# Performance work log

Hardware: AMD Instinct MI355X
Metric: run time of the kernel (lower is better)

The kernel has to match this reference:

```python
import jax, jax.numpy as jnp
import numpy as np

EMB_DIM = 1024
HID_DIM = 4096
NUM_EXPERTS = 8
TOPK = 2


def setup_inputs() -> dict:
    key = jax.random.key(0)
    ks = jax.random.split(key, 8)
    B, S, D, H, E = 4, 2048, EMB_DIM, HID_DIM, NUM_EXPERTS
    s_in = 1.0 / np.sqrt(D)
    s_hid = 1.0 / np.sqrt(H)
    x = jax.random.normal(ks[0], (B, S, D), dtype=jnp.float32)
    wr = jax.random.normal(ks[1], (D, E), dtype=jnp.float32) * s_in
    br = jnp.zeros((E,), dtype=jnp.float32)
    w1 = jax.random.normal(ks[2], (E, D, H), dtype=jnp.float32) * s_in
    b1 = jnp.zeros((E, H), dtype=jnp.float32)
    w2 = jax.random.normal(ks[3], (E, H, D), dtype=jnp.float32) * s_hid
    b2 = jnp.zeros((E, D), dtype=jnp.float32)
    return {"x": x, "wr": wr, "br": br, "w1": w1, "b1": b1, "w2": w2, "b2": b2}


def reference(x, wr, br, w1, b1, w2, b2):
    B, S, D = x.shape
    xf = x.reshape(-1, D)                                   # [T, D]
    logits = xf @ wr + br                                   # [T, E]
    probs = jax.nn.softmax(logits, axis=-1)                 # [T, E]
    _, topk_idx = jax.lax.top_k(probs, TOPK)                # [T, K]
    routed = jax.nn.one_hot(topk_idx, NUM_EXPERTS, dtype=probs.dtype).sum(axis=1)  # [T, E]
    gates = probs * routed                                  # zero for non-topk experts
    out = jnp.zeros_like(xf)
    for e in range(NUM_EXPERTS):                            # fixed small loop over experts
        h = jax.nn.relu(xf @ w1[e] + b1[e])                 # [T, H]
        y = h @ w2[e] + b2[e]                               # [T, D]
        out = out + gates[:, e:e + 1] * y
    return out.reshape(B, S, D)
```

## Files before the change

kernel.cpp:

```cpp
#include <hip/hip_runtime.h>
#include <hip/hip_bf16.h>
#include <stdint.h>


#define T_TOK 8192
#define D_DIM 1024
#define H_DIM 4096
#define NEXP  8
#define ROWCAP (T_TOK*2 + NEXP*128)

typedef short s16x8 __attribute__((ext_vector_type(8)));
typedef float f32x4 __attribute__((ext_vector_type(4)));

__device__ __forceinline__ unsigned short f2bf(float v) {
    __hip_bfloat16 b = __float2bfloat16(v);
    return __builtin_bit_cast(unsigned short, b);
}

__device__ __forceinline__ void gl_lds16(const unsigned short* g, unsigned short* l) {
    __builtin_amdgcn_global_load_lds((const __attribute__((address_space(1))) void*)g,
                                     (__attribute__((address_space(3))) void*)l, 16, 0, 0);
}


__global__ __launch_bounds__(256) void convx_kernel(const float* __restrict__ x,
                                                    unsigned short* __restrict__ xbf) {
    int i = blockIdx.x * 256 + threadIdx.x;
    float4 v = ((const float4*)x)[i];
    ushort4 o;
    o.x = f2bf(v.x); o.y = f2bf(v.y); o.z = f2bf(v.z); o.w = f2bf(v.w);
    ((ushort4*)xbf)[i] = o;
}

__global__ __launch_bounds__(256) void convt_kernel(const float* __restrict__ src,
                                                    unsigned short* __restrict__ dst,
                                                    int R, int C) {
    __shared__ float tile[32][33];
    size_t mat = (size_t)R * C;
    const float* s = src + (size_t)blockIdx.z * mat;
    unsigned short* d = dst + (size_t)blockIdx.z * mat;
    int c0 = blockIdx.x << 5, r0 = blockIdx.y << 5;
    int tx = threadIdx.x, ty = threadIdx.y;
#pragma unroll
    for (int i = 0; i < 4; i++)
        tile[ty + 8*i][tx] = s[(size_t)(r0 + ty + 8*i) * C + c0 + tx];
    __syncthreads();
#pragma unroll
    for (int i = 0; i < 4; i++)
        d[(size_t)(c0 + ty + 8*i) * R + r0 + tx] = f2bf(tile[tx][ty + 8*i]);
}


__global__ __launch_bounds__(256) void router_kernel(const float* __restrict__ x,
                                                     const float* __restrict__ wr,
                                                     const float* __restrict__ br,
                                                     int* __restrict__ counts,
                                                     int* __restrict__ te,
                                                     float* __restrict__ tg) {
    int wid = threadIdx.x >> 6, lane = threadIdx.x & 63;
    int t = blockIdx.x * 4 + wid;
    int g = lane >> 3;
    const float* xr = x + (size_t)t * D_DIM;
    float acc = 0.f;
#pragma unroll 8
    for (int j = 0; j < 128; j++)
        acc += xr[g + 8*j] * wr[lane + 64*j];
    acc += __shfl_xor(acc, 8);
    acc += __shfl_xor(acc, 16);
    acc += __shfl_xor(acc, 32);
    float lg[8];
#pragma unroll
    for (int q = 0; q < 8; q++) lg[q] = __shfl(acc, q) + br[q];
    if (lane == 0) {
        float mx = lg[0];
#pragma unroll
        for (int q = 1; q < 8; q++) mx = fmaxf(mx, lg[q]);
        float p[8], s = 0.f;
#pragma unroll
        for (int q = 0; q < 8; q++) { p[q] = __expf(lg[q] - mx); s += p[q]; }
        int i1 = 0;
#pragma unroll
        for (int q = 1; q < 8; q++) if (p[q] > p[i1]) i1 = q;
        int i2 = (i1 == 0) ? 1 : 0;
#pragma unroll
        for (int q = 0; q < 8; q++) if (q != i1 && p[q] > p[i2]) i2 = q;
        float inv = 1.f / s;
        atomicAdd(&counts[i1], 1);
        atomicAdd(&counts[i2], 1);
        te[t] = i1;          tg[t] = p[i1] * inv;
        te[T_TOK + t] = i2;  tg[T_TOK + t] = p[i2] * inv;
    }
}

__global__ void offsets_kernel(const int* __restrict__ counts, int* __restrict__ poff) {
    if (threadIdx.x == 0 && blockIdx.x == 0) {
        int acc = 0; poff[0] = 0;
#pragma unroll
        for (int e = 0; e < 8; e++) { acc += (counts[e] + 127) & ~127; poff[e + 1] = acc; }
    }
}

__global__ __launch_bounds__(256) void scatter_kernel(const int* __restrict__ te,
                                                      const float* __restrict__ tg,
                                                      int* __restrict__ counts2,
                                                      const int* __restrict__ poff,
                                                      int* __restrict__ list,
                                                      float* __restrict__ gate) {
    int i = blockIdx.x * 256 + threadIdx.x;
    if (i >= 2 * T_TOK) return;
    int e = te[i];
    int slot = atomicAdd(&counts2[e], 1);
    int gidx = poff[e] + slot;
    list[gidx] = i & (T_TOK - 1);
    gate[gidx] = tg[i];
}


__global__ __launch_bounds__(256) void ffn1_kernel(const unsigned short* __restrict__ xbf,
                                                   const unsigned short* __restrict__ w1t,
                                                   const float* __restrict__ b1,
                                                   unsigned short* __restrict__ hbuf,
                                                   const int* __restrict__ list,
                                                   const int* __restrict__ poff) {
    __shared__ unsigned short As[128 * 64];
    __shared__ unsigned short Bs[128 * 64];
    int row0 = blockIdx.x << 7;
    if (row0 >= poff[8]) return;
    int e = 0;
#pragma unroll
    for (int i = 1; i < 8; i++) e += (row0 >= poff[i]);
    const unsigned short* Bp = w1t + (size_t)e * D_DIM * H_DIM;
    int n0 = blockIdx.y << 7;
    int tid = threadIdx.x, lane = tid & 63, wid = tid >> 6;
    int wm = wid >> 1, wn = wid & 1;

    const unsigned short* asrc[4];
    const unsigned short* bsrc[4];
#pragma unroll
    for (int i = 0; i < 4; i++) {
        int lin = tid + (i << 8);
        int r = lin >> 3, kc = lin & 7;
        int tok = list[row0 + r];
        asrc[i] = xbf + (size_t)tok * D_DIM + kc * 8;
        bsrc[i] = Bp + (size_t)(n0 + r) * D_DIM + kc * 8;
    }
    f32x4 acc[4][4] = {};
    for (int k0 = 0; k0 < D_DIM; k0 += 64) {
        __syncthreads();
#pragma unroll
        for (int i = 0; i < 4; i++) {
            int lin = tid + (i << 8);
            gl_lds16(asrc[i] + k0, As + lin * 8);
            gl_lds16(bsrc[i] + k0, Bs + lin * 8);
        }
        __syncthreads();
#pragma unroll
        for (int kk = 0; kk < 64; kk += 32) {
            s16x8 af[4], bf_[4];
#pragma unroll
            for (int m = 0; m < 4; m++)
                af[m] = *(const s16x8*)(As + ((wm*64 + m*16 + (lane & 15)) * 64 + kk + (lane >> 4) * 8));
#pragma unroll
            for (int n = 0; n < 4; n++)
                bf_[n] = *(const s16x8*)(Bs + ((wn*64 + n*16 + (lane & 15)) * 64 + kk + (lane >> 4) * 8));
#pragma unroll
            for (int m = 0; m < 4; m++)
#pragma unroll
                for (int n = 0; n < 4; n++)
                    acc[m][n] = __builtin_amdgcn_mfma_f32_16x16x32_bf16(af[m], bf_[n], acc[m][n], 0, 0, 0);
        }
    }
#pragma unroll
    for (int m = 0; m < 4; m++) {
        int rbase = row0 + wm*64 + m*16 + ((lane >> 4) << 2);
#pragma unroll
        for (int n = 0; n < 4; n++) {
            int c = n0 + wn*64 + n*16 + (lane & 15);
            float bias = b1[e * H_DIM + c];
#pragma unroll
            for (int j = 0; j < 4; j++) {
                float v = fmaxf(acc[m][n][j] + bias, 0.0f);
                hbuf[(size_t)(rbase + j) * H_DIM + c] = f2bf(v);
            }
        }
    }
}

__global__ __launch_bounds__(256) void ffn2_kernel(const unsigned short* __restrict__ hbuf,
                                                   const unsigned short* __restrict__ w2t,
                                                   const float* __restrict__ b2,
                                                   float* __restrict__ out,
                                                   const int* __restrict__ list,
                                                   const float* __restrict__ gate,
                                                   const int* __restrict__ poff) {
    __shared__ unsigned short As[128 * 64];
    __shared__ unsigned short Bs[128 * 64];
    int row0 = blockIdx.x << 7;
    if (row0 >= poff[8]) return;
    int e = 0;
#pragma unroll
    for (int i = 1; i < 8; i++) e += (row0 >= poff[i]);
    const unsigned short* Bp = w2t + (size_t)e * D_DIM * H_DIM;
    int n0 = blockIdx.y << 7;
    int tid = threadIdx.x, lane = tid & 63, wid = tid >> 6;
    int wm = wid >> 1, wn = wid & 1;

    const unsigned short* asrc[4];
    const unsigned short* bsrc[4];
#pragma unroll
    for (int i = 0; i < 4; i++) {
        int lin = tid + (i << 8);
        int r = lin >> 3, kc = lin & 7;
        asrc[i] = hbuf + (size_t)(row0 + r) * H_DIM + kc * 8;
        bsrc[i] = Bp + (size_t)(n0 + r) * H_DIM + kc * 8;
    }
    f32x4 acc[4][4] = {};
    for (int k0 = 0; k0 < H_DIM; k0 += 64) {
        __syncthreads();
#pragma unroll
        for (int i = 0; i < 4; i++) {
            int lin = tid + (i << 8);
            gl_lds16(asrc[i] + k0, As + lin * 8);
            gl_lds16(bsrc[i] + k0, Bs + lin * 8);
        }
        __syncthreads();
#pragma unroll
        for (int kk = 0; kk < 64; kk += 32) {
            s16x8 af[4], bf_[4];
#pragma unroll
            for (int m = 0; m < 4; m++)
                af[m] = *(const s16x8*)(As + ((wm*64 + m*16 + (lane & 15)) * 64 + kk + (lane >> 4) * 8));
#pragma unroll
            for (int n = 0; n < 4; n++)
                bf_[n] = *(const s16x8*)(Bs + ((wn*64 + n*16 + (lane & 15)) * 64 + kk + (lane >> 4) * 8));
#pragma unroll
            for (int m = 0; m < 4; m++)
#pragma unroll
                for (int n = 0; n < 4; n++)
                    acc[m][n] = __builtin_amdgcn_mfma_f32_16x16x32_bf16(af[m], bf_[n], acc[m][n], 0, 0, 0);
        }
    }
#pragma unroll
    for (int m = 0; m < 4; m++) {
#pragma unroll
        for (int j = 0; j < 4; j++) {
            int srow = row0 + wm*64 + m*16 + ((lane >> 4) << 2) + j;
            float g = gate[srow];
            if (g != 0.0f) {
                int tok = list[srow];
#pragma unroll
                for (int n = 0; n < 4; n++) {
                    int c = n0 + wn*64 + n*16 + (lane & 15);
                    float v = g * (acc[m][n][j] + b2[e * D_DIM + c]);
                    atomicAdd(&out[(size_t)tok * D_DIM + c], v);
                }
            }
        }
    }
}


extern "C" void kernel_launch(void* const* d_in, const int* in_sizes, int n_in,
                              void* d_out, int out_size, void* d_ws, size_t ws_size,
                              hipStream_t stream) {
    const float* x  = (const float*)d_in[0];
    const float* wr = (const float*)d_in[1];
    const float* br = (const float*)d_in[2];
    const float* w1 = (const float*)d_in[3];
    const float* b1 = (const float*)d_in[4];
    const float* w2 = (const float*)d_in[5];
    const float* b2 = (const float*)d_in[6];
    float* out = (float*)d_out;
    (void)in_sizes; (void)n_in; (void)ws_size;

    char* ws = (char*)d_ws;
    size_t off = 0;
    auto alloc = [&](size_t bytes) { size_t o = off; off = (off + bytes + 1023) & ~(size_t)1023; return o; };
    size_t o_meta = alloc(256);
    size_t o_list = alloc((size_t)ROWCAP * 4);
    size_t o_gate = alloc((size_t)ROWCAP * 4);
    size_t o_te   = alloc((size_t)2 * T_TOK * 4);
    size_t o_tg   = alloc((size_t)2 * T_TOK * 4);
    size_t o_xbf  = alloc((size_t)T_TOK * D_DIM * 2);
    size_t o_w1t  = alloc((size_t)NEXP * D_DIM * H_DIM * 2);
    size_t o_w2t  = alloc((size_t)NEXP * D_DIM * H_DIM * 2);
    size_t o_h    = alloc((size_t)ROWCAP * H_DIM * 2);

    int* counts  = (int*)(ws + o_meta);
    int* counts2 = counts + 8;
    int* poff    = counts + 16;
    int* list    = (int*)(ws + o_list);
    float* gate  = (float*)(ws + o_gate);
    int* te      = (int*)(ws + o_te);
    float* tg    = (float*)(ws + o_tg);
    unsigned short* xbf = (unsigned short*)(ws + o_xbf);
    unsigned short* w1t = (unsigned short*)(ws + o_w1t);
    unsigned short* w2t = (unsigned short*)(ws + o_w2t);
    unsigned short* hbuf = (unsigned short*)(ws + o_h);

    hipMemsetAsync(ws + o_meta, 0, 256, stream);
    hipMemsetAsync(ws + o_list, 0, (size_t)ROWCAP * 4, stream);
    hipMemsetAsync(ws + o_gate, 0, (size_t)ROWCAP * 4, stream);
    hipMemsetAsync(d_out, 0, (size_t)out_size * 4, stream);

    convx_kernel<<<T_TOK * D_DIM / 4 / 256, 256, 0, stream>>>(x, xbf);
    convt_kernel<<<dim3(H_DIM / 32, D_DIM / 32, NEXP), dim3(32, 8), 0, stream>>>(w1, w1t, D_DIM, H_DIM);
    convt_kernel<<<dim3(D_DIM / 32, H_DIM / 32, NEXP), dim3(32, 8), 0, stream>>>(w2, w2t, H_DIM, D_DIM);

    router_kernel<<<T_TOK / 4, 256, 0, stream>>>(x, wr, br, counts, te, tg);
    offsets_kernel<<<1, 64, 0, stream>>>(counts, poff);
    scatter_kernel<<<(2 * T_TOK) / 256, 256, 0, stream>>>(te, tg, counts2, poff, list, gate);

    ffn1_kernel<<<dim3(ROWCAP / 128, H_DIM / 128), 256, 0, stream>>>(xbf, w1t, b1, hbuf, list, poff);
    ffn2_kernel<<<dim3(ROWCAP / 128, D_DIM / 128), 256, 0, stream>>>(hbuf, w2t, b2, out, list, gate, poff);
}
```

Measured before the change: 1.272 ms.

## Swizzle LDS tiles and replace atomic scatter with per-slot buffer plus combine

Applies an XOR swizzle to the LDS layout of the A and B tiles in both expert GEMMs, so the MFMA fragment reads avoid bank conflicts. The second GEMM no longer does atomicAdd into the output. It writes gated per-slot rows to a new fp32 buffer, and a combine kernel then sums each token's two slots. This drops the output memset and atomic contention, at the cost of an extra 64MB-scale buffer write and read plus one more launch.

```diff
diff --git a/kernel.cpp b/kernel.cpp
--- a/kernel.cpp
+++ b/kernel.cpp
@@ -20,6 +20,10 @@
 __device__ __forceinline__ void gl_lds16(const unsigned short* g, unsigned short* l) {
     __builtin_amdgcn_global_load_lds((const __attribute__((address_space(1))) void*)g,
                                      (__attribute__((address_space(3))) void*)l, 16, 0, 0);
+}
+
+__device__ __forceinline__ s16x8 lds_frag(const unsigned short* base, int row, int chunk) {
+    return *(const s16x8*)(base + row * 64 + ((chunk ^ (row & 7)) << 3));
 }
 
 
@@ -105,7 +109,8 @@
                                                       int* __restrict__ counts2,
                                                       const int* __restrict__ poff,
                                                       int* __restrict__ list,
-                                                      float* __restrict__ gate) {
+                                                      float* __restrict__ gate,
+                                                      int* __restrict__ slotof) {
     int i = blockIdx.x * 256 + threadIdx.x;
     if (i >= 2 * T_TOK) return;
     int e = te[i];
@@ -113,6 +118,7 @@
     int gidx = poff[e] + slot;
     list[gidx] = i & (T_TOK - 1);
     gate[gidx] = tg[i];
+    slotof[i] = gidx;
 }
 
 
@@ -140,9 +146,10 @@
     for (int i = 0; i < 4; i++) {
         int lin = tid + (i << 8);
         int r = lin >> 3, kc = lin & 7;
+        int sc = kc ^ (r & 7);
         int tok = list[row0 + r];
-        asrc[i] = xbf + (size_t)tok * D_DIM + kc * 8;
-        bsrc[i] = Bp + (size_t)(n0 + r) * D_DIM + kc * 8;
+        asrc[i] = xbf + (size_t)tok * D_DIM + sc * 8;
+        bsrc[i] = Bp + (size_t)(n0 + r) * D_DIM + sc * 8;
     }
     f32x4 acc[4][4] = {};
     for (int k0 = 0; k0 < D_DIM; k0 += 64) {
@@ -159,10 +166,10 @@
             s16x8 af[4], bf_[4];
 #pragma unroll
             for (int m = 0; m < 4; m++)
-                af[m] = *(const s16x8*)(As + ((wm*64 + m*16 + (lane & 15)) * 64 + kk + (lane >> 4) * 8));
+                af[m] = lds_frag(As, wm*64 + m*16 + (lane & 15), (kk >> 3) + (lane >> 4));
 #pragma unroll
             for (int n = 0; n < 4; n++)
-                bf_[n] = *(const s16x8*)(Bs + ((wn*64 + n*16 + (lane & 15)) * 64 + kk + (lane >> 4) * 8));
+                bf_[n] = lds_frag(Bs, wn*64 + n*16 + (lane & 15), (kk >> 3) + (lane >> 4));
 #pragma unroll
             for (int m = 0; m < 4; m++)
 #pragma unroll
@@ -189,8 +196,7 @@
 __global__ __launch_bounds__(256) void ffn2_kernel(const unsigned short* __restrict__ hbuf,
                                                    const unsigned short* __restrict__ w2t,
                                                    const float* __restrict__ b2,
-                                                   float* __restrict__ out,
-                                                   const int* __restrict__ list,
+                                                   float* __restrict__ ybuf,
                                                    const float* __restrict__ gate,
                                                    const int* __restrict__ poff) {
     __shared__ unsigned short As[128 * 64];
@@ -211,8 +217,9 @@
     for (int i = 0; i < 4; i++) {
         int lin = tid + (i << 8);
         int r = lin >> 3, kc = lin & 7;
-        asrc[i] = hbuf + (size_t)(row0 + r) * H_DIM + kc * 8;
-        bsrc[i] = Bp + (size_t)(n0 + r) * H_DIM + kc * 8;
+        int sc = kc ^ (r & 7);
+        asrc[i] = hbuf + (size_t)(row0 + r) * H_DIM + sc * 8;
+        bsrc[i] = Bp + (size_t)(n0 + r) * H_DIM + sc * 8;
     }
     f32x4 acc[4][4] = {};
     for (int k0 = 0; k0 < H_DIM; k0 += 64) {
@@ -229,10 +236,10 @@
             s16x8 af[4], bf_[4];
 #pragma unroll
             for (int m = 0; m < 4; m++)
-                af[m] = *(const s16x8*)(As + ((wm*64 + m*16 + (lane & 15)) * 64 + kk + (lane >> 4) * 8));
+                af[m] = lds_frag(As, wm*64 + m*16 + (lane & 15), (kk >> 3) + (lane >> 4));
 #pragma unroll
             for (int n = 0; n < 4; n++)
-                bf_[n] = *(const s16x8*)(Bs + ((wn*64 + n*16 + (lane & 15)) * 64 + kk + (lane >> 4) * 8));
+                bf_[n] = lds_frag(Bs, wn*64 + n*16 + (lane & 15), (kk >> 3) + (lane >> 4));
 #pragma unroll
             for (int m = 0; m < 4; m++)
 #pragma unroll
@@ -246,17 +253,27 @@
         for (int j = 0; j < 4; j++) {
             int srow = row0 + wm*64 + m*16 + ((lane >> 4) << 2) + j;
             float g = gate[srow];
-            if (g != 0.0f) {
-                int tok = list[srow];
-#pragma unroll
-                for (int n = 0; n < 4; n++) {
-                    int c = n0 + wn*64 + n*16 + (lane & 15);
-                    float v = g * (acc[m][n][j] + b2[e * D_DIM + c]);
-                    atomicAdd(&out[(size_t)tok * D_DIM + c], v);
-                }
+            float* yr = ybuf + (size_t)srow * D_DIM;
+#pragma unroll
+            for (int n = 0; n < 4; n++) {
+                int c = n0 + wn*64 + n*16 + (lane & 15);
+                yr[c] = g * (acc[m][n][j] + b2[e * D_DIM + c]);
             }
         }
     }
+}
+
+__global__ __launch_bounds__(256) void combine_kernel(const float* __restrict__ ybuf,
+                                                      const int* __restrict__ slotof,
+                                                      float* __restrict__ out) {
+    int t = blockIdx.x;
+    int s1 = slotof[t], s2 = slotof[T_TOK + t];
+    const float4* y1 = (const float4*)(ybuf + (size_t)s1 * D_DIM);
+    const float4* y2 = (const float4*)(ybuf + (size_t)s2 * D_DIM);
+    float4* o = (float4*)(out + (size_t)t * D_DIM);
+    int i = threadIdx.x;
+    float4 a = y1[i], b = y2[i];
+    o[i] = make_float4(a.x + b.x, a.y + b.y, a.z + b.z, a.w + b.w);
 }
 
 
@@ -271,7 +288,7 @@
     const float* w2 = (const float*)d_in[5];
     const float* b2 = (const float*)d_in[6];
     float* out = (float*)d_out;
-    (void)in_sizes; (void)n_in; (void)ws_size;
+    (void)in_sizes; (void)n_in; (void)ws_size; (void)out_size;
 
     char* ws = (char*)d_ws;
     size_t off = 0;
@@ -279,29 +296,32 @@
     size_t o_meta = alloc(256);
     size_t o_list = alloc((size_t)ROWCAP * 4);
     size_t o_gate = alloc((size_t)ROWCAP * 4);
+    size_t o_slot = alloc((size_t)2 * T_TOK * 4);
     size_t o_te   = alloc((size_t)2 * T_TOK * 4);
     size_t o_tg   = alloc((size_t)2 * T_TOK * 4);
     size_t o_xbf  = alloc((size_t)T_TOK * D_DIM * 2);
     size_t o_w1t  = alloc((size_t)NEXP * D_DIM * H_DIM * 2);
     size_t o_w2t  = alloc((size_t)NEXP * D_DIM * H_DIM * 2);
     size_t o_h    = alloc((size_t)ROWCAP * H_DIM * 2);
+    size_t o_y    = alloc((size_t)ROWCAP * D_DIM * 4);
 
     int* counts  = (int*)(ws + o_meta);
     int* counts2 = counts + 8;
     int* poff    = counts + 16;
     int* list    = (int*)(ws + o_list);
     float* gate  = (float*)(ws + o_gate);
+    int* slotof  = (int*)(ws + o_slot);
     int* te      = (int*)(ws + o_te);
     float* tg    = (float*)(ws + o_tg);
     unsigned short* xbf = (unsigned short*)(ws + o_xbf);
     unsigned short* w1t = (unsigned short*)(ws + o_w1t);
     unsigned short* w2t = (unsigned short*)(ws + o_w2t);
     unsigned short* hbuf = (unsigned short*)(ws + o_h);
+    float* ybuf  = (float*)(ws + o_y);
 
     hipMemsetAsync(ws + o_meta, 0, 256, stream);
     hipMemsetAsync(ws + o_list, 0, (size_t)ROWCAP * 4, stream);
     hipMemsetAsync(ws + o_gate, 0, (size_t)ROWCAP * 4, stream);
-    hipMemsetAsync(d_out, 0, (size_t)out_size * 4, stream);
 
     convx_kernel<<<T_TOK * D_DIM / 4 / 256, 256, 0, stream>>>(x, xbf);
     convt_kernel<<<dim3(H_DIM / 32, D_DIM / 32, NEXP), dim3(32, 8), 0, stream>>>(w1, w1t, D_DIM, H_DIM);
@@ -309,8 +329,10 @@
 
     router_kernel<<<T_TOK / 4, 256, 0, stream>>>(x, wr, br, counts, te, tg);
     offsets_kernel<<<1, 64, 0, stream>>>(counts, poff);
-    scatter_kernel<<<(2 * T_TOK) / 256, 256, 0, stream>>>(te, tg, counts2, poff, list, gate);
+    scatter_kernel<<<(2 * T_TOK) / 256, 256, 0, stream>>>(te, tg, counts2, poff, list, gate, slotof);
 
     ffn1_kernel<<<dim3(ROWCAP / 128, H_DIM / 128), 256, 0, stream>>>(xbf, w1t, b1, hbuf, list, poff);
-    ffn2_kernel<<<dim3(ROWCAP / 128, D_DIM / 128), 256, 0, stream>>>(hbuf, w2t, b2, out, list, gate, poff);
-}
+    ffn2_kernel<<<dim3(ROWCAP / 128, D_DIM / 128), 256, 0, stream>>>(hbuf, w2t, b2, ybuf, gate, poff);
+
+    combine_kernel<<<T_TOK, 256, 0, stream>>>(ybuf, slotof, out);
+}
```

Result: faster. 1.109 ms (-12.8%).
